# Optimization experiments

Measured on AMD Instinct MI355X. Metric: run time of the kernel, lower is better.

## Reference

```python
import jax, jax.numpy as jnp
import numpy as np

B, IN, OUT, K, RES, WDIM = 8, 512, 512, 3, 64, 512
CONV_RC = 1.0 / np.sqrt(K * K * IN).astype(np.float32)   # gain*lrmul/sqrt(fan_in), gain=lrmul=1
DENSE_RC = 1.0 / np.sqrt(WDIM).astype(np.float32)
CONV_INIT_STD = float(CONV_RC)   # init_std = he_std / lrmul
DENSE_INIT_STD = float(DENSE_RC)


def setup_inputs() -> dict:
    key = jax.random.key(0)
    k1, k2, k3, k4 = jax.random.split(key, 4)
    return {
        "x": jax.random.normal(k1, (B, IN, RES, RES), jnp.float32),
        "y": jax.random.normal(k2, (B, WDIM), jnp.float32),
        "w": jax.random.normal(k3, (K, K, IN, OUT), jnp.float32) * CONV_INIT_STD,
        "w_mod": jax.random.normal(k4, (WDIM, IN), jnp.float32) * DENSE_INIT_STD,
        "b_mod": jnp.zeros((IN,), jnp.float32),
    }


def reference(x, y, w, w_mod, b_mod):
    # equalized-lr runtime scaling
    w_s = w * CONV_RC                                   # [K,K,IN,OUT]
    # style: s = dense(y) + bias + 1
    s = y @ (w_mod * DENSE_RC) + b_mod + 1.0            # [B,IN]
    # modulate per-sample weights
    ww = w_s[None] * s[:, None, None, :, None]          # [B,K,K,IN,OUT]
    # demodulate
    d = jax.lax.rsqrt(jnp.sum(jnp.square(ww), axis=(1, 2, 3)) + 1e-8)  # [B,OUT]
    ww = ww * d[:, None, None, None, :]
    # fused modconv: grouped conv with groups = B
    xr = x.reshape(1, B * IN, RES, RES)
    wk = jnp.transpose(ww, (1, 2, 3, 0, 4)).reshape(K, K, IN, B * OUT)
    out = jax.lax.conv_general_dilated(
        xr, wk, window_strides=(1, 1), padding="SAME",
        dimension_numbers=("NCHW", "HWIO", "NCHW"),
        feature_group_count=B)
    return out.reshape(B, OUT, RES, RES)
```

## Files before the change

### kernel.cpp

```cpp
#include <hip/hip_runtime.h>
#include <hip/hip_bf16.h>

typedef __bf16 bf16x8 __attribute__((ext_vector_type(8)));
typedef float f32x4 __attribute__((ext_vector_type(4)));
typedef unsigned short u16;
typedef u16 u16x8 __attribute__((ext_vector_type(8)));

#define DENSE_RC 0.0441941738f
#define CONV_RC  0.0147313913f

__device__ inline u16 f2bf(float v) {
  union { float f; unsigned u; } x; x.f = v;
  unsigned r = x.u + 0x7fffu + ((x.u >> 16) & 1u);
  return (u16)(r >> 16);
}

__device__ inline void gload16(const void* g, void* l) {
  __builtin_amdgcn_global_load_lds(
      (const __attribute__((address_space(1))) unsigned int*)g,
      (__attribute__((address_space(3))) unsigned int*)l, 16, 0, 0);
}

__global__ void style_k(const float* __restrict__ y, const float* __restrict__ wm,
                        const float* __restrict__ bm, float* __restrict__ s) {
  const int tid = threadIdx.x, lane = tid & 63, wv = tid >> 6;
  const int idx = blockIdx.x * 64 + lane;
  const int b = idx >> 9, i = idx & 511;
  const float* yb = y + b * 512;
  float acc = 0.f;
  const int j0 = wv * 128;
#pragma unroll 8
  for (int j = j0; j < j0 + 128; ++j) acc += yb[j] * wm[j * 512 + i];
  __shared__ float red[4][64];
  red[wv][lane] = acc;
  __syncthreads();
  if (wv == 0) {
    float a = red[0][lane] + red[1][lane] + red[2][lane] + red[3][lane];
    s[idx] = a * DENSE_RC + bm[i] + 1.0f;
  }
}

__global__ void wsq_k(const float* __restrict__ w, float* __restrict__ wsq) {
  const int idx = blockIdx.x * 256 + threadIdx.x;
  float a = 0.f;
#pragma unroll
  for (int t = 0; t < 9; ++t) { float v = w[(size_t)t * 262144 + idx]; a += v * v; }
  wsq[idx] = a;
}

__global__ void demod_k(const float* __restrict__ s, const float* __restrict__ wsq,
                        float* __restrict__ dmd) {
  const int tid = threadIdx.x, lane = tid & 63, wv = tid >> 6;
  const int idx = blockIdx.x * 64 + lane;
  const int b = idx >> 9, o = idx & 511;
  const float* sb = s + b * 512;
  float a = 0.f;
  const int i0 = wv * 128;
#pragma unroll 4
  for (int i = i0; i < i0 + 128; ++i) { float sv = sb[i]; a += sv * sv * wsq[i * 512 + o]; }
  __shared__ float red[4][64];
  red[wv][lane] = a;
  __syncthreads();
  if (wv == 0) {
    float t = red[0][lane] + red[1][lane] + red[2][lane] + red[3][lane];
    dmd[idx] = rsqrtf(t * (CONV_RC * CONV_RC) + 1e-8f);
  }
}

__global__ void modw_k(const float* __restrict__ w, const float* __restrict__ s,
                       const float* __restrict__ dmd, u16* __restrict__ wwb) {
  const int blk = blockIdx.x;
  const int ob = blk & 7, ib = (blk >> 3) & 15, t = blk >> 7;
  __shared__ float lw[32][65];
  const int tid = threadIdx.x;
#pragma unroll
  for (int k = 0; k < 8; ++k) {
    const int e = tid + k * 256;
    const int i = e >> 6, o = e & 63;
    lw[i][o] = w[(size_t)t * 262144 + (size_t)(ib * 32 + i) * 512 + ob * 64 + o];
  }
  __syncthreads();
  const int oo = tid >> 2, q = tid & 3;
  const int ii0 = q * 8;
  for (int b = 0; b < 8; ++b) {
    const float f = CONV_RC * dmd[b * 512 + ob * 64 + oo];
    u16x8 pk;
#pragma unroll
    for (int j = 0; j < 8; ++j)
      pk[j] = f2bf(lw[ii0 + j][oo] * s[b * 512 + ib * 32 + ii0 + j] * f);
    *(u16x8*)(wwb + ((size_t)(b * 9 + t) * 512 + ob * 64 + oo) * 512 + ib * 32 + ii0) = pk;
  }
}

__global__ void border_k(u16* __restrict__ xpad) {
  const int idx = blockIdx.x * 256 + threadIdx.x;
  const int chunk = idx & 63;
  const int p = (idx >> 6) % 260;
  const int b = idx / (260 * 64);
  int row, col;
  if (p < 66)       { row = 0;       col = p; }
  else if (p < 132) { row = 65;      col = p - 66; }
  else if (p < 196) { row = p - 131; col = 0; }
  else              { row = p - 195; col = 65; }
  u16x8 z = {0, 0, 0, 0, 0, 0, 0, 0};
  *(u16x8*)(xpad + ((size_t)(b * 66 + row) * 66 + col) * 512 + chunk * 8) = z;
}

__global__ void fill_k(const float* __restrict__ x, u16* __restrict__ xpad) {
  const int blk = blockIdx.x;
  const int ib = blk & 3, hh = (blk >> 2) & 63, b = blk >> 8;
  __shared__ float lx[128][65];
  const int tid = threadIdx.x;
#pragma unroll
  for (int k = 0; k < 2; ++k) {
    const int u = tid + k * 256;
    const int i = u >> 2, w0 = (u & 3) * 16;
    const float* src = x + (size_t)((b * 512 + ib * 128 + i) * 64 + hh) * 64 + w0;
    float tmp[16];
    ((float4*)tmp)[0] = ((const float4*)src)[0];
    ((float4*)tmp)[1] = ((const float4*)src)[1];
    ((float4*)tmp)[2] = ((const float4*)src)[2];
    ((float4*)tmp)[3] = ((const float4*)src)[3];
#pragma unroll
    for (int j = 0; j < 16; ++j) lx[i][w0 + j] = tmp[j];
  }
  __syncthreads();
  const int c = tid >> 2, q = tid & 3;
  const size_t base = ((size_t)(b * 66 + hh + 1) * 66 + (c + 1)) * 512 + ib * 128;
#pragma unroll
  for (int k = 0; k < 4; ++k) {
    const int irow = k * 32 + q * 8;
    u16x8 pk;
#pragma unroll
    for (int j = 0; j < 8; ++j) pk[j] = f2bf(lx[irow + j][c]);
    *(u16x8*)(xpad + base + irow) = pk;
  }
}

__global__ __launch_bounds__(256, 2) void conv_k(const u16* __restrict__ xpad,
                                                 const u16* __restrict__ wwb,
                                                 float* __restrict__ out) {
  __shared__ __align__(1024) char SM[79104];
  int blk = (int)blockIdx.x;
  blk = ((blk & 7) << 6) | (blk >> 3);
  const int pt = blk & 7, ot = (blk >> 3) & 7, b = blk >> 6;
  const int tid = threadIdx.x;
  const int lane = tid & 63, wv = tid >> 6;
  const int rA = lane >> 4, cA = lane & 15;
  const int h0 = pt * 8;

  const size_t wwbase = (size_t)(b * 9) * 262144 + (size_t)ot * 64 * 512;
  const size_t xbase  = (size_t)(b * 66 + h0) * (66 * 512);

  const u16* aw[9];  char* dw[9];
  const u16* ax[11]; char* dx[11];
#pragma unroll
  for (int r = 0; r < 9; ++r) {
    const int cc = tid + r * 256;
    const int lc = cc ^ ((cc >> 3) & 3);
    const int i8 = lc & 3, o = (lc >> 2) & 63, t = lc >> 8;
    aw[r] = wwb + wwbase + (size_t)t * 262144 + o * 512 + i8 * 8;
    dw[r] = SM + cc * 16;
  }
#pragma unroll
  for (int r = 0; r < 11; ++r) {
    const int c2 = tid + r * 256;
    const int lc = c2 ^ ((c2 >> 3) & 3);
    const int i8 = lc & 3, rc = lc >> 2;
    ax[r] = xpad + xbase + (size_t)rc * 512 + i8 * 8;
    dx[r] = SM + 36864 + c2 * 16;
  }
  const bool extra = (tid < 80);

  f32x4 acc[4][8];
#pragma unroll
  for (int i = 0; i < 4; ++i)
#pragma unroll
    for (int j = 0; j < 8; ++j) acc[i][j] = (f32x4){0.f, 0.f, 0.f, 0.f};

  const char* Ab = SM + ((cA * 64 + rA * 16) ^ ((cA << 3) & 0x30));

  for (int kb = 0; kb < 16; ++kb) {
#pragma unroll
    for (int r = 0; r < 9; ++r) gload16(aw[r], dw[r]);
#pragma unroll
    for (int r = 0; r < 10; ++r) gload16(ax[r], dx[r]);
    if (extra) gload16(ax[10], dx[10]);
    asm volatile("s_waitcnt vmcnt(0)" ::: "memory");
    __syncthreads();

#pragma unroll
    for (int t = 0; t < 9; ++t) {
      const int ty = t / 3, tx = t % 3;
      bf16x8 af[4];
#pragma unroll
      for (int mi = 0; mi < 4; ++mi)
        af[mi] = *(const bf16x8*)(Ab + t * 4096 + mi * 1024);
#pragma unroll
      for (int hf = 0; hf < 2; ++hf) {
        const int rct = (2 * wv + ty + hf) * 66 + cA + tx;
        const char* Bt = SM + 36864 + ((rct * 64 + rA * 16) ^ ((rct << 3) & 0x30));
        bf16x8 bfr[4];
#pragma unroll
        for (int n = 0; n < 4; ++n)
          bfr[n] = *(const bf16x8*)(Bt + n * 1024);
#pragma unroll
        for (int mi = 0; mi < 4; ++mi)
#pragma unroll
          for (int n = 0; n < 4; ++n)
            acc[mi][hf * 4 + n] = __builtin_amdgcn_mfma_f32_16x16x32_bf16(
                af[mi], bfr[n], acc[mi][hf * 4 + n], 0, 0, 0);
      }
    }
    __syncthreads();

#pragma unroll
    for (int r = 0; r < 9; ++r) aw[r] += 32;
#pragma unroll
    for (int r = 0; r < 11; ++r) ax[r] += 32;
  }

  const int hb = h0 + 2 * wv;
#pragma unroll
  for (int mi = 0; mi < 4; ++mi)
#pragma unroll
    for (int ni = 0; ni < 8; ++ni) {
      const int h = hb + (ni >> 2);
      const int wc = (ni & 3) * 16 + cA;
#pragma unroll
      for (int r = 0; r < 4; ++r) {
        const int o = ot * 64 + mi * 16 + rA * 4 + r;
        out[((size_t)(b * 512 + o) * 64 + h) * 64 + wc] = acc[mi][ni][r];
      }
    }
}

extern "C" void kernel_launch(void* const* d_in, const int* in_sizes, int n_in,
                              void* d_out, int out_size, void* d_ws, size_t ws_size,
                              hipStream_t stream) {
  const float* x     = (const float*)d_in[0];
  const float* y     = (const float*)d_in[1];
  const float* w     = (const float*)d_in[2];
  const float* w_mod = (const float*)d_in[3];
  const float* b_mod = (const float*)d_in[4];
  float* out = (float*)d_out;

  char* ws = (char*)d_ws;
  float* s    = (float*)(ws);
  float* dmd  = (float*)(ws + 16384);
  float* wsq  = (float*)(ws + 32768);
  u16*   wwb  = (u16*)(ws + 32768 + 1048576);
  u16*   xpad = (u16*)(ws + 32768 + 1048576 + 37748736);

  style_k<<<64, 256, 0, stream>>>(y, w_mod, b_mod, s);
  wsq_k<<<1024, 256, 0, stream>>>(w, wsq);
  demod_k<<<64, 256, 0, stream>>>(s, wsq, dmd);
  modw_k<<<1152, 256, 0, stream>>>(w, s, dmd, wwb);
  border_k<<<520, 256, 0, stream>>>(xpad);
  fill_k<<<2048, 256, 0, stream>>>(x, xpad);
  conv_k<<<512, 256, 0, stream>>>(xpad, wwb, out);
}
```

Measured before the change: 166.4 us.

## Double-buffer LDS tiles in conv kernel to overlap loads with MFMA

Doubles the shared-memory allocation so the next K-block's weight and input tiles are fetched with global_load_lds while MFMAs run on the current buffer. This removes the stall where every iteration waited for its loads before computing. The cost is occupancy: launch bounds drop from 2 to 1 block per CU because of the roughly 156KB LDS footprint, which gives up the latency hiding that two resident blocks provided. Load addressing is also simplified to a per-thread swizzle with fixed strides.

```diff
diff --git a/kernel.cpp b/kernel.cpp
--- a/kernel.cpp
+++ b/kernel.cpp
@@ -137,10 +137,10 @@
   }
 }
 
-__global__ __launch_bounds__(256, 2) void conv_k(const u16* __restrict__ xpad,
+__global__ __launch_bounds__(256, 1) void conv_k(const u16* __restrict__ xpad,
                                                  const u16* __restrict__ wwb,
                                                  float* __restrict__ out) {
-  __shared__ __align__(1024) char SM[79104];
+  __shared__ __align__(1024) char SM[159744];
   int blk = (int)blockIdx.x;
   blk = ((blk & 7) << 6) | (blk >> 3);
   const int pt = blk & 7, ot = (blk >> 3) & 7, b = blk >> 6;
@@ -152,43 +152,41 @@
   const size_t wwbase = (size_t)(b * 9) * 262144 + (size_t)ot * 64 * 512;
   const size_t xbase  = (size_t)(b * 66 + h0) * (66 * 512);
 
-  const u16* aw[9];  char* dw[9];
-  const u16* ax[11]; char* dx[11];
-#pragma unroll
-  for (int r = 0; r < 9; ++r) {
-    const int cc = tid + r * 256;
-    const int lc = cc ^ ((cc >> 3) & 3);
-    const int i8 = lc & 3, o = (lc >> 2) & 63, t = lc >> 8;
-    aw[r] = wwb + wwbase + (size_t)t * 262144 + o * 512 + i8 * 8;
-    dw[r] = SM + cc * 16;
-  }
-#pragma unroll
-  for (int r = 0; r < 11; ++r) {
-    const int c2 = tid + r * 256;
-    const int lc = c2 ^ ((c2 >> 3) & 3);
-    const int i8 = lc & 3, rc = lc >> 2;
-    ax[r] = xpad + xbase + (size_t)rc * 512 + i8 * 8;
-    dx[r] = SM + 36864 + c2 * 16;
-  }
+  const int tidswz = tid ^ ((tid >> 3) & 3);
+  const u16* aw[9];
+  const u16* ax[11];
+#pragma unroll
+  for (int r = 0; r < 9; ++r)
+    aw[r] = wwb + wwbase + (size_t)r * 262144 + ((tidswz >> 2) & 63) * 512 + (tidswz & 3) * 8;
+#pragma unroll
+  for (int r = 0; r < 11; ++r)
+    ax[r] = xpad + xbase + (size_t)((tidswz >> 2) + r * 64) * 512 + (tidswz & 3) * 8;
   const bool extra = (tid < 80);
 
+  auto stage = [&](int ofs) {
+#pragma unroll
+    for (int r = 0; r < 9; ++r)
+      gload16(aw[r], SM + ofs + tid * 16 + r * 4096);
+#pragma unroll
+    for (int r = 0; r < 10; ++r)
+      gload16(ax[r], SM + ofs + 36864 + tid * 16 + r * 4096);
+    if (extra) gload16(ax[10], SM + ofs + 36864 + tid * 16 + 40960);
+#pragma unroll
+    for (int r = 0; r < 9; ++r) aw[r] += 32;
+#pragma unroll
+    for (int r = 0; r < 11; ++r) ax[r] += 32;
+  };
+
   f32x4 acc[4][8];
 #pragma unroll
   for (int i = 0; i < 4; ++i)
 #pragma unroll
     for (int j = 0; j < 8; ++j) acc[i][j] = (f32x4){0.f, 0.f, 0.f, 0.f};
 
-  const char* Ab = SM + ((cA * 64 + rA * 16) ^ ((cA << 3) & 0x30));
-
-  for (int kb = 0; kb < 16; ++kb) {
-#pragma unroll
-    for (int r = 0; r < 9; ++r) gload16(aw[r], dw[r]);
-#pragma unroll
-    for (int r = 0; r < 10; ++r) gload16(ax[r], dx[r]);
-    if (extra) gload16(ax[10], dx[10]);
-    asm volatile("s_waitcnt vmcnt(0)" ::: "memory");
-    __syncthreads();
-
+  const int AbOff = (cA * 64 + rA * 16) ^ ((cA << 3) & 0x30);
+
+  auto compute = [&](int ofs) {
+    const char* Ab = SM + ofs + AbOff;
 #pragma unroll
     for (int t = 0; t < 9; ++t) {
       const int ty = t / 3, tx = t % 3;
@@ -199,7 +197,7 @@
 #pragma unroll
       for (int hf = 0; hf < 2; ++hf) {
         const int rct = (2 * wv + ty + hf) * 66 + cA + tx;
-        const char* Bt = SM + 36864 + ((rct * 64 + rA * 16) ^ ((rct << 3) & 0x30));
+        const char* Bt = SM + ofs + 36864 + ((rct * 64 + rA * 16) ^ ((rct << 3) & 0x30));
         bf16x8 bfr[4];
 #pragma unroll
         for (int n = 0; n < 4; ++n)
@@ -212,13 +210,21 @@
                 af[mi], bfr[n], acc[mi][hf * 4 + n], 0, 0, 0);
       }
     }
+  };
+
+  stage(0);
+  asm volatile("s_waitcnt vmcnt(0)" ::: "memory");
+  __syncthreads();
+
+  int cofs = 0, nofs = 79872;
+  for (int kb = 0; kb < 15; ++kb) {
+    stage(nofs);
+    compute(cofs);
+    asm volatile("s_waitcnt vmcnt(0)" ::: "memory");
     __syncthreads();
-
-#pragma unroll
-    for (int r = 0; r < 9; ++r) aw[r] += 32;
-#pragma unroll
-    for (int r = 0; r < 11; ++r) ax[r] += 32;
-  }
+    const int t = cofs; cofs = nofs; nofs = t;
+  }
+  compute(cofs);
 
   const int hb = h0 + 2 * wv;
 #pragma unroll
```

Result: slower. 171.2 us (+2.9%).

## Enlarge conv tile to 128 output channels with 8-wave blocks

Applied to the files above, without the earlier changes.

The implicit-GEMM conv block now covers 128 output channels instead of 64, using 512 threads arranged as 2 output-channel waves by 4 row waves. Each staged input tile is therefore reused by twice as many output channels, which roughly halves the redundant x loads. The LDS swizzle and load addressing are simplified to a single base pointer with stride offsets. Block ordering now puts the channel tile innermost. In exchange, the grid shrinks to 256 blocks and LDS use grows to about 116 KB per block, which may cut occupancy and leave fewer blocks to fill all CUs.

```diff
diff --git a/kernel.cpp b/kernel.cpp
--- a/kernel.cpp
+++ b/kernel.cpp
@@ -137,39 +137,24 @@
   }
 }
 
-__global__ __launch_bounds__(256, 2) void conv_k(const u16* __restrict__ xpad,
+__global__ __launch_bounds__(512, 2) void conv_k(const u16* __restrict__ xpad,
                                                  const u16* __restrict__ wwb,
                                                  float* __restrict__ out) {
-  __shared__ __align__(1024) char SM[79104];
-  int blk = (int)blockIdx.x;
-  blk = ((blk & 7) << 6) | (blk >> 3);
-  const int pt = blk & 7, ot = (blk >> 3) & 7, b = blk >> 6;
+  __shared__ __align__(1024) char SM[115968];
+  const int blk = (int)blockIdx.x;
+  const int pt = blk >> 5, b = (blk >> 2) & 7, ot = blk & 3;
   const int tid = threadIdx.x;
   const int lane = tid & 63, wv = tid >> 6;
   const int rA = lane >> 4, cA = lane & 15;
+  const int wo = wv & 1, wr = wv >> 1;
   const int h0 = pt * 8;
 
-  const size_t wwbase = (size_t)(b * 9) * 262144 + (size_t)ot * 64 * 512;
+  const size_t wwbase = (size_t)b * 9 * 262144 + (size_t)ot * 65536;
   const size_t xbase  = (size_t)(b * 66 + h0) * (66 * 512);
 
-  const u16* aw[9];  char* dw[9];
-  const u16* ax[11]; char* dx[11];
-#pragma unroll
-  for (int r = 0; r < 9; ++r) {
-    const int cc = tid + r * 256;
-    const int lc = cc ^ ((cc >> 3) & 3);
-    const int i8 = lc & 3, o = (lc >> 2) & 63, t = lc >> 8;
-    aw[r] = wwb + wwbase + (size_t)t * 262144 + o * 512 + i8 * 8;
-    dw[r] = SM + cc * 16;
-  }
-#pragma unroll
-  for (int r = 0; r < 11; ++r) {
-    const int c2 = tid + r * 256;
-    const int lc = c2 ^ ((c2 >> 3) & 3);
-    const int i8 = lc & 3, rc = lc >> 2;
-    ax[r] = xpad + xbase + (size_t)rc * 512 + i8 * 8;
-    dx[r] = SM + 36864 + c2 * 16;
-  }
+  const int tidswz = tid ^ ((tid >> 3) & 3);
+  const u16* awb = wwb + wwbase + (tidswz >> 2) * 512 + (tidswz & 3) * 8;
+  const u16* axb = xpad + xbase + (size_t)(tidswz >> 2) * 512 + (tidswz & 3) * 8;
   const bool extra = (tid < 80);
 
   f32x4 acc[4][8];
@@ -178,14 +163,17 @@
 #pragma unroll
     for (int j = 0; j < 8; ++j) acc[i][j] = (f32x4){0.f, 0.f, 0.f, 0.f};
 
-  const char* Ab = SM + ((cA * 64 + rA * 16) ^ ((cA << 3) & 0x30));
+  const int AbO = ((wo * 4096 + cA * 64 + rA * 16) ^ (((cA >> 1) & 3) << 4));
 
   for (int kb = 0; kb < 16; ++kb) {
 #pragma unroll
-    for (int r = 0; r < 9; ++r) gload16(aw[r], dw[r]);
-#pragma unroll
-    for (int r = 0; r < 10; ++r) gload16(ax[r], dx[r]);
-    if (extra) gload16(ax[10], dx[10]);
+    for (int r = 0; r < 9; ++r)
+      gload16(awb + (size_t)r * 262144, SM + tid * 16 + r * 8192);
+#pragma unroll
+    for (int r = 0; r < 5; ++r)
+      gload16(axb + (size_t)r * 65536, SM + 73728 + tid * 16 + r * 8192);
+    if (extra) gload16(axb + 5 * 65536, SM + 73728 + tid * 16 + 40960);
+    awb += 32; axb += 32;
     asm volatile("s_waitcnt vmcnt(0)" ::: "memory");
     __syncthreads();
 
@@ -195,11 +183,11 @@
       bf16x8 af[4];
 #pragma unroll
       for (int mi = 0; mi < 4; ++mi)
-        af[mi] = *(const bf16x8*)(Ab + t * 4096 + mi * 1024);
+        af[mi] = *(const bf16x8*)(SM + AbO + t * 8192 + mi * 1024);
 #pragma unroll
       for (int hf = 0; hf < 2; ++hf) {
-        const int rct = (2 * wv + ty + hf) * 66 + cA + tx;
-        const char* Bt = SM + 36864 + ((rct * 64 + rA * 16) ^ ((rct << 3) & 0x30));
+        const int rct = (2 * wr + ty + hf) * 66 + tx + cA;
+        const char* Bt = SM + 73728 + ((rct * 64 + rA * 16) ^ (((rct >> 1) & 3) << 4));
         bf16x8 bfr[4];
 #pragma unroll
         for (int n = 0; n < 4; ++n)
@@ -213,14 +201,9 @@
       }
     }
     __syncthreads();
-
-#pragma unroll
-    for (int r = 0; r < 9; ++r) aw[r] += 32;
-#pragma unroll
-    for (int r = 0; r < 11; ++r) ax[r] += 32;
-  }
-
-  const int hb = h0 + 2 * wv;
+  }
+
+  const int hb = h0 + 2 * wr;
 #pragma unroll
   for (int mi = 0; mi < 4; ++mi)
 #pragma unroll
@@ -229,7 +212,7 @@
       const int wc = (ni & 3) * 16 + cA;
 #pragma unroll
       for (int r = 0; r < 4; ++r) {
-        const int o = ot * 64 + mi * 16 + rA * 4 + r;
+        const int o = ot * 128 + wo * 64 + mi * 16 + rA * 4 + r;
         out[((size_t)(b * 512 + o) * 64 + h) * 64 + wc] = acc[mi][ni][r];
       }
     }
@@ -258,5 +241,5 @@
   modw_k<<<1152, 256, 0, stream>>>(w, s, dmd, wwb);
   border_k<<<520, 256, 0, stream>>>(xpad);
   fill_k<<<2048, 256, 0, stream>>>(x, xpad);
-  conv_k<<<512, 256, 0, stream>>>(xpad, wwb, out);
-}
+  conv_k<<<256, 512, 0, stream>>>(xpad, wwb, out);
+}
```

New measurement: 167.1 us. Within noise of the previous version (+0.5%).
